# Optimization experiments

Hardware: AMD Instinct MI355X
Metric: run time of the kernel (lower is better)

Reference implementation:

```python
import jax, jax.numpy as jnp
import numpy as np

B, N, C = 2, 4096, 1024
H, WIN = 16, 20
D = C // H

def setup_inputs() -> dict:
    key = jax.random.key(0)
    ks = jax.random.split(key, 9)
    s = 1.0 / np.sqrt(C)
    d = {"q": jax.random.normal(ks[0], (B, N, C), jnp.float32)}
    for i, name in enumerate(["Wq", "Wk", "Wv", "Wo"]):
        d[name + "_w"] = jax.random.normal(ks[1 + 2 * i], (C, C), jnp.float32) * s
        d[name + "_b"] = jax.random.normal(ks[2 + 2 * i], (C,), jnp.float32) * 0.01
    return d

def reference(q, Wq_w, Wq_b, Wk_w, Wk_b, Wv_w, Wv_b, Wo_w, Wo_b):
    b, n, c = q.shape
    w2 = WIN // 2  # half window = 10
    def proj(x, w, bias):
        return (x @ w.T + bias).reshape(b, n, H, D).transpose(0, 2, 1, 3)  # [B,H,N,D]
    Q = proj(q, Wq_w, Wq_b)
    K = proj(q, Wk_w, Wk_b)
    V = proj(q, Wv_w, Wv_b)
    off = jnp.arange(-w2, w2 + 1)                       # [Wn] = 21 offsets
    pos = jnp.arange(n)[:, None] + off[None, :]         # [N, Wn] key index per query
    valid = (pos >= 0) & (pos < n)                      # edge clipping == torch start/end slicing
    idx = jnp.clip(pos, 0, n - 1)
    Kw = K[:, :, idx, :]                                # [B,H,N,Wn,D] gathered key windows
    Vw = V[:, :, idx, :]
    scale = jnp.sqrt(jnp.float32(D))
    scores = jnp.einsum('bhnd,bhnwd->bhnw', Q, Kw) / scale
    scores = jnp.where(valid[None, None], scores, -jnp.inf)
    probs = jax.nn.softmax(scores, axis=-1)             # invalid slots get exactly 0
    out = jnp.einsum('bhnw,bhnwd->bhnd', probs, Vw)
    out = out.transpose(0, 2, 1, 3).reshape(b, n, c)
    out = out @ Wo_w.T + Wo_b
    # torch returns attn_probs of the LAST loop iteration i=N-1: window [N-1-w2, N), size w2+1
    attn_last = probs[:, :, -1:, : w2 + 1]              # [B,H,1,11]
    return (out, attn_last)
```

## Files before the change

kernel.cpp:

```cpp
#include <hip/hip_runtime.h>
#include <hip/hip_bf16.h>

#define Bb 2
#define Nn 4096
#define Cc 1024
#define Hh 16
#define Dd 64
#define Mm (Bb*Nn)
#define W2 10
#define WINSZ 21

typedef __attribute__((ext_vector_type(8))) short  bf16x8s;
typedef __attribute__((ext_vector_type(4))) float  f32x4;
typedef __attribute__((ext_vector_type(4))) unsigned short us4;

#define AS1 __attribute__((address_space(1)))
#define AS3 __attribute__((address_space(3)))

__device__ __forceinline__ unsigned short f2bf(float f) {
  unsigned int u = __float_as_uint(f);
  u += 0x7FFFu + ((u >> 16) & 1u);
  return (unsigned short)(u >> 16);
}
__device__ __forceinline__ float bflo(unsigned int u) { return __uint_as_float(u << 16); }
__device__ __forceinline__ float bfhi(unsigned int u) { return __uint_as_float(u & 0xFFFF0000u); }

__device__ __forceinline__ us4 cvt4(float4 v) {
  us4 o;
  o.x = f2bf(v.x); o.y = f2bf(v.y); o.z = f2bf(v.z); o.w = f2bf(v.w);
  return o;
}

__global__ __launch_bounds__(256) void cvt_all(const float4* __restrict__ q,
                                               const float4* __restrict__ wq,
                                               const float4* __restrict__ wk,
                                               const float4* __restrict__ wv,
                                               const float4* __restrict__ wo,
                                               const float* __restrict__ bq,
                                               const float* __restrict__ bk,
                                               const float* __restrict__ bv,
                                               us4* __restrict__ qb4,
                                               us4* __restrict__ wqkv4,
                                               us4* __restrict__ wo4,
                                               float* __restrict__ bqkv) {
  const int NQ = 2097152, NW = 262144, TOT = NQ + 4 * NW;
  const int gid = blockIdx.x * 256 + threadIdx.x;
  const int stride = gridDim.x * 256;
  for (int i = gid; i < TOT; i += stride) {
    if (i < NQ) {
      qb4[i] = cvt4(q[i]);
    } else {
      int j = i - NQ;
      int r = j >> 18, k = j & (NW - 1);
      if (r == 0)      wqkv4[k]          = cvt4(wq[k]);
      else if (r == 1) wqkv4[NW + k]     = cvt4(wk[k]);
      else if (r == 2) wqkv4[2 * NW + k] = cvt4(wv[k]);
      else             wo4[k]            = cvt4(wo[k]);
    }
  }
  if (gid < 3072) {
    float v = (gid < 1024) ? bq[gid] : (gid < 2048) ? bk[gid - 1024] : bv[gid - 2048];
    bqkv[gid] = v;
  }
}

template<bool OUT_BF16>
__global__ __launch_bounds__(512) void gemm_k32(const unsigned short* __restrict__ A,
                                                const unsigned short* __restrict__ Bm,
                                                const float* __restrict__ bias,
                                                void* __restrict__ Cout,
                                                int N) {
  constexpr int K = 1024, NT = 32;
  __shared__ unsigned short lds[3][12288];

  const int tid = threadIdx.x, wid = tid >> 6, lane = tid & 63;
  const int wm = wid >> 2, wn = wid & 3;

  const int nwg = gridDim.x, cpx = nwg >> 3, bid = blockIdx.x;
  const int swz = (bid & 7) * cpx + (bid >> 3);
  const int nbn = N >> 8;
  const int m0 = (swz / nbn) << 7, n0 = (swz % nbn) << 8;

  const unsigned short* aS  = A  + (size_t)(m0 + wid * 16 + (lane >> 2)) * K + (lane & 3) * 8;
  const unsigned short* bS0 = Bm + (size_t)(n0 + wid * 32 + (lane >> 2)) * K + (lane & 3) * 8;
  const unsigned short* bS1 = bS0 + (size_t)16 * K;
  const int dA = wid * 512, dB0 = 4096 + wid * 1024, dB1 = 4096 + wid * 1024 + 512;

#define STG(bf, kt) do {                                                                      \
    const size_t ko = (size_t)(kt) * 32;                                                      \
    __builtin_amdgcn_global_load_lds((AS1 const void*)(aS  + ko), (AS3 void*)(&lds[bf][dA ]), 16, 0, 0); \
    __builtin_amdgcn_global_load_lds((AS1 const void*)(bS0 + ko), (AS3 void*)(&lds[bf][dB0]), 16, 0, 0); \
    __builtin_amdgcn_global_load_lds((AS1 const void*)(bS1 + ko), (AS3 void*)(&lds[bf][dB1]), 16, 0, 0); \
  } while (0)

  int aoff[4], boff[4];
#pragma unroll
  for (int f = 0; f < 4; ++f) {
    aoff[f] = (wm * 64 + f * 16 + (lane & 15)) * 32 + (lane >> 4) * 8;
    boff[f] = 4096 + (wn * 64 + f * 16 + (lane & 15)) * 32 + (lane >> 4) * 8;
  }

  f32x4 acc[4][4] = {};

  STG(0, 0);
  STG(1, 1);
  asm volatile("s_waitcnt vmcnt(3)" ::: "memory");
  __builtin_amdgcn_sched_barrier(0);
  __builtin_amdgcn_s_barrier();
  __builtin_amdgcn_sched_barrier(0);

#pragma unroll 4
  for (int t = 0; t < NT; ++t) {
    const int cur = t % 3;
    if (t + 2 < NT) STG((t + 2) % 3, t + 2);

    const unsigned short* L = &lds[cur][0];
    bf16x8s a[4], b[4];
#pragma unroll
    for (int f = 0; f < 4; ++f) a[f] = *(const bf16x8s*)(L + aoff[f]);
#pragma unroll
    for (int f = 0; f < 4; ++f) b[f] = *(const bf16x8s*)(L + boff[f]);
    __builtin_amdgcn_s_setprio(1);
#pragma unroll
    for (int fm = 0; fm < 4; ++fm)
#pragma unroll
      for (int fn = 0; fn < 4; ++fn)
        acc[fm][fn] = __builtin_amdgcn_mfma_f32_16x16x32_bf16(a[fm], b[fn], acc[fm][fn], 0, 0, 0);
    __builtin_amdgcn_s_setprio(0);

    if (t + 1 < NT) {
      if (t + 2 < NT) asm volatile("s_waitcnt vmcnt(3)" ::: "memory");
      else            asm volatile("s_waitcnt vmcnt(0)" ::: "memory");
      __builtin_amdgcn_sched_barrier(0);
      __builtin_amdgcn_s_barrier();
      __builtin_amdgcn_sched_barrier(0);
    }
  }
#undef STG

  const int r0 = m0 + wm * 64 + (lane >> 4) * 4;
  const int c0 = n0 + wn * 64 + (lane & 15);
#pragma unroll
  for (int fm = 0; fm < 4; ++fm) {
#pragma unroll
    for (int fn = 0; fn < 4; ++fn) {
      const int col = c0 + fn * 16;
      const float bv = bias[col];
#pragma unroll
      for (int r = 0; r < 4; ++r) {
        const int row = r0 + fm * 16 + r;
        const float v = acc[fm][fn][r] + bv;
        if (OUT_BF16)
          ((unsigned short*)Cout)[(size_t)row * N + col] = f2bf(v);
        else
          ((float*)Cout)[(size_t)row * N + col] = v;
      }
    }
  }
}

#define TN 128
#define KVROWS (TN + 2 * W2)

__global__ void attn_kernel(const unsigned short* __restrict__ QKV,
                            unsigned short* __restrict__ AO,
                            float* __restrict__ attn_last) {
  __shared__ uint4 Kl[KVROWS * 8];
  __shared__ uint4 Vl[KVROWS * 8];

  const int nt = Nn / TN;
  const int bid = blockIdx.x;
  const int tile = bid & (nt - 1);
  const int bh = bid / nt;
  const int h = bh & (Hh - 1), b = bh / Hh;
  const int n0 = tile * TN;
  const int tid = threadIdx.x;

  for (int idx = tid; idx < KVROWS * 8; idx += 256) {
    const int r = idx >> 3, c = idx & 7;
    const int pos = n0 - W2 + r;
    uint4 kv = make_uint4(0, 0, 0, 0), vv = make_uint4(0, 0, 0, 0);
    if (pos >= 0 && pos < Nn) {
      const uint4* row = (const uint4*)(QKV + (size_t)(b * Nn + pos) * 3072);
      kv = row[128 + h * 8 + c];
      vv = row[256 + h * 8 + c];
    }
    const int slot = c ^ (r & 7);
    Kl[r * 8 + slot] = kv;
    Vl[r * 8 + slot] = vv;
  }
  __syncthreads();

  const int row  = tid >> 1;
  const int half = tid & 1;
  const int n = n0 + row;
  const size_t m = (size_t)b * Nn + n;

  const uint4* qrow = (const uint4*)(QKV + m * 3072) + h * 8 + half * 4;
  const uint4 qd0 = qrow[0], qd1 = qrow[1], qd2 = qrow[2], qd3 = qrow[3];

  float p[WINSZ];
#pragma unroll
  for (int w = 0; w < WINSZ; ++w) p[w] = 0.f;

#pragma unroll
  for (int c = 0; c < 4; ++c) {
    const uint4 qv = (c == 0) ? qd0 : (c == 1) ? qd1 : (c == 2) ? qd2 : qd3;
    const float q0 = bflo(qv.x), q1 = bfhi(qv.x);
    const float q2 = bflo(qv.y), q3 = bfhi(qv.y);
    const float q4 = bflo(qv.z), q5 = bfhi(qv.z);
    const float q6 = bflo(qv.w), q7 = bfhi(qv.w);
#pragma unroll 7
    for (int w = 0; w < WINSZ; ++w) {
      const int r = row + w;
      const uint4 v = Kl[r * 8 + ((half * 4 + c) ^ (r & 7))];
      float a0 = q0 * bflo(v.x);
      float a1 = q1 * bfhi(v.x);
      a0 += q2 * bflo(v.y);
      a1 += q3 * bfhi(v.y);
      a0 += q4 * bflo(v.z);
      a1 += q5 * bfhi(v.z);
      a0 += q6 * bflo(v.w);
      a1 += q7 * bfhi(v.w);
      p[w] += a0 + a1;
    }
  }

#pragma unroll
  for (int w = 0; w < WINSZ; ++w) {
    float t = p[w];
    t += __shfl_xor(t, 1, 64);
    const int pos = n - W2 + w;
    p[w] = (pos < 0 || pos >= Nn) ? -1e30f : t * 0.125f;
  }
  float mx = p[0];
#pragma unroll
  for (int w = 1; w < WINSZ; ++w) mx = fmaxf(mx, p[w]);
  float sum = 0.f;
#pragma unroll
  for (int w = 0; w < WINSZ; ++w) { p[w] = __expf(p[w] - mx); sum += p[w]; }
  const float inv = 1.0f / sum;

  if (n == Nn - 1 && half == 0) {
#pragma unroll
    for (int w = 0; w <= W2; ++w)
      attn_last[(b * Hh + h) * (W2 + 1) + w] = p[w] * inv;
  }

  uint4* orow = (uint4*)(AO + m * Cc + h * Dd) + half * 4;
#pragma unroll
  for (int c = 0; c < 4; ++c) {
    float o0 = 0.f, o1 = 0.f, o2 = 0.f, o3 = 0.f;
    float o4 = 0.f, o5 = 0.f, o6 = 0.f, o7 = 0.f;
#pragma unroll 7
    for (int w = 0; w < WINSZ; ++w) {
      const int r = row + w;
      const uint4 v = Vl[r * 8 + ((half * 4 + c) ^ (r & 7))];
      const float pw = p[w];
      o0 += pw * bflo(v.x);
      o1 += pw * bfhi(v.x);
      o2 += pw * bflo(v.y);
      o3 += pw * bfhi(v.y);
      o4 += pw * bflo(v.z);
      o5 += pw * bfhi(v.z);
      o6 += pw * bflo(v.w);
      o7 += pw * bfhi(v.w);
    }
    unsigned int d0 = (unsigned int)f2bf(o0 * inv) | ((unsigned int)f2bf(o1 * inv) << 16);
    unsigned int d1 = (unsigned int)f2bf(o2 * inv) | ((unsigned int)f2bf(o3 * inv) << 16);
    unsigned int d2 = (unsigned int)f2bf(o4 * inv) | ((unsigned int)f2bf(o5 * inv) << 16);
    unsigned int d3 = (unsigned int)f2bf(o6 * inv) | ((unsigned int)f2bf(o7 * inv) << 16);
    orow[c] = make_uint4(d0, d1, d2, d3);
  }
}

extern "C" void kernel_launch(void* const* d_in, const int* in_sizes, int n_in,
                              void* d_out, int out_size, void* d_ws, size_t ws_size,
                              hipStream_t stream) {
  const float* q    = (const float*)d_in[0];
  const float* Wq_w = (const float*)d_in[1];
  const float* Wq_b = (const float*)d_in[2];
  const float* Wk_w = (const float*)d_in[3];
  const float* Wk_b = (const float*)d_in[4];
  const float* Wv_w = (const float*)d_in[5];
  const float* Wv_b = (const float*)d_in[6];
  const float* Wo_w = (const float*)d_in[7];
  const float* Wo_b = (const float*)d_in[8];
  float* out = (float*)d_out;
  float* attn_last = out + (size_t)Mm * Cc;

  char* ws = (char*)d_ws;
  unsigned short* qb   = (unsigned short*)(ws);
  unsigned short* Wqkv = (unsigned short*)(ws + 16777216);
  unsigned short* Wo16 = (unsigned short*)(ws + 16777216 + 6291456);
  float*          bqkv = (float*)(ws + 25165824);
  unsigned short* QKV  = (unsigned short*)(ws + 25182208);
  unsigned short* AO   = (unsigned short*)(ws + 75513856);

  cvt_all<<<2048, 256, 0, stream>>>((const float4*)q,
                                    (const float4*)Wq_w, (const float4*)Wk_w,
                                    (const float4*)Wv_w, (const float4*)Wo_w,
                                    Wq_b, Wk_b, Wv_b,
                                    (us4*)qb, (us4*)Wqkv, (us4*)Wo16, bqkv);

  {
    dim3 grid((Mm / 128) * (3072 / 256));
    gemm_k32<true><<<grid, 512, 0, stream>>>(qb, Wqkv, bqkv, (void*)QKV, 3072);
  }

  {
    dim3 grid(Bb * Hh * (Nn / TN));
    attn_kernel<<<grid, 256, 0, stream>>>(QKV, AO, attn_last);
  }

  {
    dim3 grid((Mm / 128) * (Cc / 256));
    gemm_k32<false><<<grid, 512, 0, stream>>>(AO, Wo16, Wo_b, (void*)out, Cc);
  }
}
```

Measured before the change: 145.9 us.

## Replace GEMM with 256x256-tile, K64, XOR-swizzled, 8-phase pipelined kernel

Rewrites both projection GEMMs to use 256x256 output tiles with K-step 64, double-buffered 128KB LDS staging and XOR-swizzled chunk placement to avoid bank conflicts. The main loop interleaves partial LDS reads, global-to-LDS prefetches and MFMA bursts in an 8-phase schedule with barriers and priority hints. Larger tiles aim to raise arithmetic intensity and MFMA utilisation. The cost is more accumulator registers, fewer workgroups (the output GEMM drops to 128 blocks, fewer than the CU count), and many barriers per iteration.

After: 145.8 us. About the same (-0.0%).

```diff
diff --git a/kernel.cpp b/kernel.cpp
--- a/kernel.cpp
+++ b/kernel.cpp
@@ -65,83 +65,99 @@
 }
 
 template<bool OUT_BF16>
-__global__ __launch_bounds__(512) void gemm_k32(const unsigned short* __restrict__ A,
-                                                const unsigned short* __restrict__ Bm,
-                                                const float* __restrict__ bias,
-                                                void* __restrict__ Cout,
-                                                int N) {
-  constexpr int K = 1024, NT = 32;
-  __shared__ unsigned short lds[3][12288];
+__global__ __launch_bounds__(512) void gemm8p(const unsigned short* __restrict__ A,
+                                              const unsigned short* __restrict__ Bm,
+                                              const float* __restrict__ bias,
+                                              void* __restrict__ Cout,
+                                              int N) {
+  constexpr int K = 1024;
+  __shared__ unsigned short lds[65536];
 
   const int tid = threadIdx.x, wid = tid >> 6, lane = tid & 63;
   const int wm = wid >> 2, wn = wid & 3;
 
   const int nwg = gridDim.x, cpx = nwg >> 3, bid = blockIdx.x;
   const int swz = (bid & 7) * cpx + (bid >> 3);
-  const int nbn = N >> 8;
-  const int m0 = (swz / nbn) << 7, n0 = (swz % nbn) << 8;
-
-  const unsigned short* aS  = A  + (size_t)(m0 + wid * 16 + (lane >> 2)) * K + (lane & 3) * 8;
-  const unsigned short* bS0 = Bm + (size_t)(n0 + wid * 32 + (lane >> 2)) * K + (lane & 3) * 8;
-  const unsigned short* bS1 = bS0 + (size_t)16 * K;
-  const int dA = wid * 512, dB0 = 4096 + wid * 1024, dB1 = 4096 + wid * 1024 + 512;
-
-#define STG(bf, kt) do {                                                                      \
-    const size_t ko = (size_t)(kt) * 32;                                                      \
-    __builtin_amdgcn_global_load_lds((AS1 const void*)(aS  + ko), (AS3 void*)(&lds[bf][dA ]), 16, 0, 0); \
-    __builtin_amdgcn_global_load_lds((AS1 const void*)(bS0 + ko), (AS3 void*)(&lds[bf][dB0]), 16, 0, 0); \
-    __builtin_amdgcn_global_load_lds((AS1 const void*)(bS1 + ko), (AS3 void*)(&lds[bf][dB1]), 16, 0, 0); \
-  } while (0)
-
-  int aoff[4], boff[4];
-#pragma unroll
-  for (int f = 0; f < 4; ++f) {
-    aoff[f] = (wm * 64 + f * 16 + (lane & 15)) * 32 + (lane >> 4) * 8;
-    boff[f] = 4096 + (wn * 64 + f * 16 + (lane & 15)) * 32 + (lane >> 4) * 8;
-  }
-
-  f32x4 acc[4][4] = {};
-
-  STG(0, 0);
-  STG(1, 1);
-  asm volatile("s_waitcnt vmcnt(3)" ::: "memory");
-  __builtin_amdgcn_sched_barrier(0);
-  __builtin_amdgcn_s_barrier();
-  __builtin_amdgcn_sched_barrier(0);
-
-#pragma unroll 4
-  for (int t = 0; t < NT; ++t) {
-    const int cur = t % 3;
-    if (t + 2 < NT) STG((t + 2) % 3, t + 2);
-
-    const unsigned short* L = &lds[cur][0];
-    bf16x8s a[4], b[4];
-#pragma unroll
-    for (int f = 0; f < 4; ++f) a[f] = *(const bf16x8s*)(L + aoff[f]);
-#pragma unroll
-    for (int f = 0; f < 4; ++f) b[f] = *(const bf16x8s*)(L + boff[f]);
-    __builtin_amdgcn_s_setprio(1);
-#pragma unroll
-    for (int fm = 0; fm < 4; ++fm)
-#pragma unroll
-      for (int fn = 0; fn < 4; ++fn)
-        acc[fm][fn] = __builtin_amdgcn_mfma_f32_16x16x32_bf16(a[fm], b[fn], acc[fm][fn], 0, 0, 0);
-    __builtin_amdgcn_s_setprio(0);
-
-    if (t + 1 < NT) {
-      if (t + 2 < NT) asm volatile("s_waitcnt vmcnt(3)" ::: "memory");
-      else            asm volatile("s_waitcnt vmcnt(0)" ::: "memory");
-      __builtin_amdgcn_sched_barrier(0);
-      __builtin_amdgcn_s_barrier();
-      __builtin_amdgcn_sched_barrier(0);
-    }
-  }
-#undef STG
-
-  const int r0 = m0 + wm * 64 + (lane >> 4) * 4;
+  constexpr int NBM = Mm / 256;
+  const int m0 = (swz % NBM) << 8, n0 = (swz / NBM) << 8;
+
+  const int rbase = wid * 8 + (lane >> 3);
+  const int cst = ((lane & 7) ^ (lane >> 3)) * 8;
+  const unsigned short* aP0 = A  + (size_t)(m0 + rbase) * K + cst;
+  const unsigned short* aP1 = aP0 + (size_t)128 * K;
+  const unsigned short* bP0 = Bm + (size_t)(n0 + rbase) * K + cst;
+  const unsigned short* bP1 = bP0 + (size_t)128 * K;
+
+  const int awb = wm * 8192 + (lane & 15) * 64;
+  const int bwb = 16384 + (wn >> 1) * 8192 + (wn & 1) * 4096 + (lane & 15) * 64;
+  const int chs0 = (((lane >> 4)) ^ (lane & 7)) * 8;
+  const int chs1 = ((4 + (lane >> 4)) ^ (lane & 7)) * 8;
+
+  f32x4 acc[8][4] = {};
+  bf16x8s breg[4][2], areg[2][2];
+
+#define GL(sp, off) __builtin_amdgcn_global_load_lds((AS1 const void*)(sp), (AS3 void*)(&lds[off]), 16, 0, 0)
+#define STGA(d,h,kt) do { const unsigned short* _s = ((h) ? aP1 : aP0) + (size_t)(kt) * 64; \
+    GL(_s,                   (d)*32768 + (h)*8192 +        wid*512); \
+    GL(_s + (size_t)64 * K,  (d)*32768 + (h)*8192 + 4096 + wid*512); } while (0)
+#define STGB(d,h,kt) do { const unsigned short* _s = ((h) ? bP1 : bP0) + (size_t)(kt) * 64; \
+    GL(_s,                   (d)*32768 + 16384 + (h)*8192 +        wid*512); \
+    GL(_s + (size_t)64 * K,  (d)*32768 + 16384 + (h)*8192 + 4096 + wid*512); } while (0)
+#define LDB(d) do { _Pragma("unroll") for (int fn = 0; fn < 4; ++fn) { \
+    breg[fn][0] = *(const bf16x8s*)(&lds[(d)*32768 + bwb + fn*1024 + chs0]); \
+    breg[fn][1] = *(const bf16x8s*)(&lds[(d)*32768 + bwb + fn*1024 + chs1]); } } while (0)
+#define LDA(d,q) do { _Pragma("unroll") for (int u = 0; u < 2; ++u) { \
+    areg[u][0] = *(const bf16x8s*)(&lds[(d)*32768 + awb + ((q)*2+u)*1024 + chs0]); \
+    areg[u][1] = *(const bf16x8s*)(&lds[(d)*32768 + awb + ((q)*2+u)*1024 + chs1]); } } while (0)
+#define MF16(q) do { _Pragma("unroll") for (int u = 0; u < 2; ++u) _Pragma("unroll") for (int fn = 0; fn < 4; ++fn) { \
+    acc[(q)*2+u][fn] = __builtin_amdgcn_mfma_f32_16x16x32_bf16(areg[u][0], breg[fn][0], acc[(q)*2+u][fn], 0, 0, 0); \
+    acc[(q)*2+u][fn] = __builtin_amdgcn_mfma_f32_16x16x32_bf16(areg[u][1], breg[fn][1], acc[(q)*2+u][fn], 0, 0, 0); } } while (0)
+#define SB __builtin_amdgcn_sched_barrier(0)
+#define BAR __builtin_amdgcn_s_barrier()
+#define LGKM0 asm volatile("s_waitcnt lgkmcnt(0)" ::: "memory")
+#define PRIO1 __builtin_amdgcn_s_setprio(1)
+#define PRIO0 __builtin_amdgcn_s_setprio(0)
+
+  STGA(0,0,0); STGA(0,1,0); STGB(0,0,0); STGB(0,1,0);
+  STGA(1,0,1); STGA(1,1,1); STGB(1,0,1); STGB(1,1,1);
+  asm volatile("s_waitcnt vmcnt(8)" ::: "memory");
+  SB; BAR; SB;
+
+#pragma unroll 1
+  for (int j = 0; j < 8; ++j) {
+    const int tA1 = 2*j + 1;
+    const int t0  = (2*j + 2) & 15;
+    const int tB1 = (2*j + 3) & 15;
+    LDB(0); LDA(0,0); STGA(1,0,tA1);          SB; BAR; LGKM0; SB;
+    PRIO1; MF16(0); PRIO0; SB; BAR; SB;
+    LDA(0,1); STGA(1,1,tA1); STGB(0,0,t0);    SB; BAR; LGKM0; SB;
+    PRIO1; MF16(1); PRIO0; SB; BAR; SB;
+    LDA(0,2); STGB(0,1,t0);                   SB; BAR; LGKM0; SB;
+    PRIO1; MF16(2); PRIO0; SB; BAR; SB;
+    LDA(0,3);                                 SB; BAR; LGKM0; SB;
+    PRIO1; MF16(3); PRIO0; SB;
+    asm volatile("s_waitcnt vmcnt(4)" ::: "memory"); SB; BAR; SB;
+    LDB(1); LDA(1,0); STGA(0,0,t0);           SB; BAR; LGKM0; SB;
+    PRIO1; MF16(0); PRIO0; SB; BAR; SB;
+    LDA(1,1); STGA(0,1,t0); STGB(1,0,tB1);    SB; BAR; LGKM0; SB;
+    PRIO1; MF16(1); PRIO0; SB; BAR; SB;
+    LDA(1,2); STGB(1,1,tB1);                  SB; BAR; LGKM0; SB;
+    PRIO1; MF16(2); PRIO0; SB; BAR; SB;
+    LDA(1,3);                                 SB; BAR; LGKM0; SB;
+    PRIO1; MF16(3); PRIO0; SB;
+    asm volatile("s_waitcnt vmcnt(4)" ::: "memory"); SB; BAR; SB;
+  }
+#undef GL
+#undef STGA
+#undef STGB
+#undef LDB
+#undef LDA
+#undef MF16
+
+  const int r0 = m0 + wm * 128 + (lane >> 4) * 4;
   const int c0 = n0 + wn * 64 + (lane & 15);
 #pragma unroll
-  for (int fm = 0; fm < 4; ++fm) {
+  for (int fm = 0; fm < 8; ++fm) {
 #pragma unroll
     for (int fn = 0; fn < 4; ++fn) {
       const int col = c0 + fn * 16;
@@ -304,8 +320,8 @@
                                     (us4*)qb, (us4*)Wqkv, (us4*)Wo16, bqkv);
 
   {
-    dim3 grid((Mm / 128) * (3072 / 256));
-    gemm_k32<true><<<grid, 512, 0, stream>>>(qb, Wqkv, bqkv, (void*)QKV, 3072);
+    dim3 grid((Mm / 256) * (3072 / 256));
+    gemm8p<true><<<grid, 512, 0, stream>>>(qb, Wqkv, bqkv, (void*)QKV, 3072);
   }
 
   {
@@ -314,7 +330,7 @@
   }
 
   {
-    dim3 grid((Mm / 128) * (Cc / 256));
-    gemm_k32<false><<<grid, 512, 0, stream>>>(AO, Wo16, Wo_b, (void*)out, Cc);
-  }
-}
+    dim3 grid((Mm / 256) * (Cc / 256));
+    gemm8p<false><<<grid, 512, 0, stream>>>(AO, Wo16, Wo_b, (void*)out, Cc);
+  }
+}
```

## Switch GEMMs to 128x128 tiles with 256 threads and XOR-swizzled LDS layout

Applied to the files above, without the earlier changes.

Both projection GEMMs move from 128x256 tiles on 512-thread blocks to 128x128 tiles on 256-thread blocks, with a 2x2 wave layout and M-major block ordering. The global-to-LDS staging now uses an XOR swizzle on the 16-byte column group, and the fragment reads apply the same swizzle, to cut LDS bank conflicts. The ring-buffer indices are tracked incrementally with unroll 1 instead of modulo arithmetic. Smaller tiles give more blocks and smaller LDS use per block, at the cost of less operand reuse per block.

New measurement: 151.6 us. 1.04x slower.

```diff
diff --git a/kernel.cpp b/kernel.cpp
--- a/kernel.cpp
+++ b/kernel.cpp
@@ -65,54 +65,59 @@
 }
 
 template<bool OUT_BF16>
-__global__ __launch_bounds__(512) void gemm_k32(const unsigned short* __restrict__ A,
-                                                const unsigned short* __restrict__ Bm,
-                                                const float* __restrict__ bias,
-                                                void* __restrict__ Cout,
-                                                int N) {
+__global__ __launch_bounds__(256) void gemm_mb(const unsigned short* __restrict__ A,
+                                               const unsigned short* __restrict__ Bm,
+                                               const float* __restrict__ bias,
+                                               void* __restrict__ Cout,
+                                               int N) {
   constexpr int K = 1024, NT = 32;
-  __shared__ unsigned short lds[3][12288];
+  __shared__ unsigned short lds[3][8192];
 
   const int tid = threadIdx.x, wid = tid >> 6, lane = tid & 63;
-  const int wm = wid >> 2, wn = wid & 3;
+  const int wm = wid >> 1, wn = wid & 1;
 
   const int nwg = gridDim.x, cpx = nwg >> 3, bid = blockIdx.x;
   const int swz = (bid & 7) * cpx + (bid >> 3);
-  const int nbn = N >> 8;
-  const int m0 = (swz / nbn) << 7, n0 = (swz % nbn) << 8;
-
-  const unsigned short* aS  = A  + (size_t)(m0 + wid * 16 + (lane >> 2)) * K + (lane & 3) * 8;
-  const unsigned short* bS0 = Bm + (size_t)(n0 + wid * 32 + (lane >> 2)) * K + (lane & 3) * 8;
-  const unsigned short* bS1 = bS0 + (size_t)16 * K;
-  const int dA = wid * 512, dB0 = 4096 + wid * 1024, dB1 = 4096 + wid * 1024 + 512;
-
-#define STG(bf, kt) do {                                                                      \
-    const size_t ko = (size_t)(kt) * 32;                                                      \
-    __builtin_amdgcn_global_load_lds((AS1 const void*)(aS  + ko), (AS3 void*)(&lds[bf][dA ]), 16, 0, 0); \
-    __builtin_amdgcn_global_load_lds((AS1 const void*)(bS0 + ko), (AS3 void*)(&lds[bf][dB0]), 16, 0, 0); \
-    __builtin_amdgcn_global_load_lds((AS1 const void*)(bS1 + ko), (AS3 void*)(&lds[bf][dB1]), 16, 0, 0); \
+  constexpr int NBM = Mm / 128;
+  const int m0 = (swz % NBM) << 7, n0 = (swz / NBM) << 7;
+
+  const int srow = tid >> 2;
+  const int g = (tid & 3) ^ (srow & 3) ^ ((srow >> 2) & 3);
+  const unsigned short* aS0 = A  + (size_t)(m0 + srow) * K + g * 8;
+  const unsigned short* aS1 = aS0 + (size_t)64 * K;
+  const unsigned short* bS0 = Bm + (size_t)(n0 + srow) * K + g * 8;
+  const unsigned short* bS1 = bS0 + (size_t)64 * K;
+  const int d0 = wid * 512;
+
+#define STG(bf, kt) do {                                                                    \
+    const size_t ko = (size_t)(kt) * 32;                                                    \
+    __builtin_amdgcn_global_load_lds((AS1 const void*)(aS0 + ko), (AS3 void*)(&lds[bf][       d0]), 16, 0, 0); \
+    __builtin_amdgcn_global_load_lds((AS1 const void*)(aS1 + ko), (AS3 void*)(&lds[bf][2048 + d0]), 16, 0, 0); \
+    __builtin_amdgcn_global_load_lds((AS1 const void*)(bS0 + ko), (AS3 void*)(&lds[bf][4096 + d0]), 16, 0, 0); \
+    __builtin_amdgcn_global_load_lds((AS1 const void*)(bS1 + ko), (AS3 void*)(&lds[bf][6144 + d0]), 16, 0, 0); \
   } while (0)
 
+  const int slot8 = (((lane >> 4) ^ (lane & 3) ^ ((lane >> 2) & 3))) * 8;
   int aoff[4], boff[4];
 #pragma unroll
   for (int f = 0; f < 4; ++f) {
-    aoff[f] = (wm * 64 + f * 16 + (lane & 15)) * 32 + (lane >> 4) * 8;
-    boff[f] = 4096 + (wn * 64 + f * 16 + (lane & 15)) * 32 + (lane >> 4) * 8;
+    aoff[f] = (wm * 64 + f * 16 + (lane & 15)) * 32 + slot8;
+    boff[f] = 4096 + (wn * 64 + f * 16 + (lane & 15)) * 32 + slot8;
   }
 
   f32x4 acc[4][4] = {};
 
   STG(0, 0);
   STG(1, 1);
-  asm volatile("s_waitcnt vmcnt(3)" ::: "memory");
+  asm volatile("s_waitcnt vmcnt(4)" ::: "memory");
   __builtin_amdgcn_sched_barrier(0);
   __builtin_amdgcn_s_barrier();
   __builtin_amdgcn_sched_barrier(0);
 
-#pragma unroll 4
+  int cur = 0, stg = 2;
+#pragma unroll 1
   for (int t = 0; t < NT; ++t) {
-    const int cur = t % 3;
-    if (t + 2 < NT) STG((t + 2) % 3, t + 2);
+    if (t + 2 < NT) STG(stg, t + 2);
 
     const unsigned short* L = &lds[cur][0];
     bf16x8s a[4], b[4];
@@ -129,12 +134,14 @@
     __builtin_amdgcn_s_setprio(0);
 
     if (t + 1 < NT) {
-      if (t + 2 < NT) asm volatile("s_waitcnt vmcnt(3)" ::: "memory");
+      if (t + 2 < NT) asm volatile("s_waitcnt vmcnt(4)" ::: "memory");
       else            asm volatile("s_waitcnt vmcnt(0)" ::: "memory");
       __builtin_amdgcn_sched_barrier(0);
       __builtin_amdgcn_s_barrier();
       __builtin_amdgcn_sched_barrier(0);
     }
+    cur = (cur == 2) ? 0 : cur + 1;
+    stg = (stg == 2) ? 0 : stg + 1;
   }
 #undef STG
 
@@ -304,8 +311,8 @@
                                     (us4*)qb, (us4*)Wqkv, (us4*)Wo16, bqkv);
 
   {
-    dim3 grid((Mm / 128) * (3072 / 256));
-    gemm_k32<true><<<grid, 512, 0, stream>>>(qb, Wqkv, bqkv, (void*)QKV, 3072);
+    dim3 grid((Mm / 128) * (3072 / 128));
+    gemm_mb<true><<<grid, 256, 0, stream>>>(qb, Wqkv, bqkv, (void*)QKV, 3072);
   }
 
   {
@@ -314,7 +321,7 @@
   }
 
   {
-    dim3 grid((Mm / 128) * (Cc / 256));
-    gemm_k32<false><<<grid, 512, 0, stream>>>(AO, Wo16, Wo_b, (void*)out, Cc);
-  }
-}
+    dim3 grid((Mm / 128) * (Cc / 128));
+    gemm_mb<false><<<grid, 256, 0, stream>>>(AO, Wo16, Wo_b, (void*)out, Cc);
+  }
+}
```

## Swizzle GEMM LDS layout and split attention rows across four threads

Applied to the files above, without the earlier changes.

The GEMM's global-to-LDS staging now uses an XOR swizzle on the 16-byte chunk index, with matching swizzled read offsets. This is meant to cut LDS bank conflicts when fragments are loaded, and it also changes how the B tile rows are laid out in LDS. The attention kernel goes from 256 to 512 threads, with each query row split across four lanes instead of two and an extra shuffle reduction. This raises parallelism and lowers per-thread register pressure, at the cost of more redundant softmax work and shuffles.

Result: faster. 140.0 us (-4.0%).

```diff
diff --git a/kernel.cpp b/kernel.cpp
--- a/kernel.cpp
+++ b/kernel.cpp
@@ -81,10 +81,12 @@
   const int nbn = N >> 8;
   const int m0 = (swz / nbn) << 7, n0 = (swz % nbn) << 8;
 
-  const unsigned short* aS  = A  + (size_t)(m0 + wid * 16 + (lane >> 2)) * K + (lane & 3) * 8;
-  const unsigned short* bS0 = Bm + (size_t)(n0 + wid * 32 + (lane >> 2)) * K + (lane & 3) * 8;
-  const unsigned short* bS1 = bS0 + (size_t)16 * K;
-  const int dA = wid * 512, dB0 = 4096 + wid * 1024, dB1 = 4096 + wid * 1024 + 512;
+  const int srow = wid * 16 + (lane >> 2);
+  const int g8 = ((lane & 3) ^ ((lane >> 3) & 3)) * 8;
+  const unsigned short* aS  = A  + (size_t)(m0 + srow) * K + g8;
+  const unsigned short* bS0 = Bm + (size_t)(n0 + srow) * K + g8;
+  const unsigned short* bS1 = Bm + (size_t)(n0 + 128 + srow) * K + g8;
+  const int dA = wid * 512, dB0 = 4096 + wid * 512, dB1 = 8192 + wid * 512;
 
 #define STG(bf, kt) do {                                                                      \
     const size_t ko = (size_t)(kt) * 32;                                                      \
@@ -93,11 +95,12 @@
     __builtin_amdgcn_global_load_lds((AS1 const void*)(bS1 + ko), (AS3 void*)(&lds[bf][dB1]), 16, 0, 0); \
   } while (0)
 
+  const int slot8 = ((lane >> 4) ^ (((lane & 15) >> 1) & 3)) * 8;
   int aoff[4], boff[4];
 #pragma unroll
   for (int f = 0; f < 4; ++f) {
-    aoff[f] = (wm * 64 + f * 16 + (lane & 15)) * 32 + (lane >> 4) * 8;
-    boff[f] = 4096 + (wn * 64 + f * 16 + (lane & 15)) * 32 + (lane >> 4) * 8;
+    aoff[f] = (wm * 64 + f * 16 + (lane & 15)) * 32 + slot8;
+    boff[f] = 4096 + (wn * 64 + f * 16 + (lane & 15)) * 32 + slot8;
   }
 
   f32x4 acc[4][4] = {};
@@ -162,9 +165,9 @@
 #define TN 128
 #define KVROWS (TN + 2 * W2)
 
-__global__ void attn_kernel(const unsigned short* __restrict__ QKV,
-                            unsigned short* __restrict__ AO,
-                            float* __restrict__ attn_last) {
+__global__ __launch_bounds__(512) void attn_kernel(const unsigned short* __restrict__ QKV,
+                                                   unsigned short* __restrict__ AO,
+                                                   float* __restrict__ attn_last) {
   __shared__ uint4 Kl[KVROWS * 8];
   __shared__ uint4 Vl[KVROWS * 8];
 
@@ -176,7 +179,7 @@
   const int n0 = tile * TN;
   const int tid = threadIdx.x;
 
-  for (int idx = tid; idx < KVROWS * 8; idx += 256) {
+  for (int idx = tid; idx < KVROWS * 8; idx += 512) {
     const int r = idx >> 3, c = idx & 7;
     const int pos = n0 - W2 + r;
     uint4 kv = make_uint4(0, 0, 0, 0), vv = make_uint4(0, 0, 0, 0);
@@ -191,21 +194,21 @@
   }
   __syncthreads();
 
-  const int row  = tid >> 1;
-  const int half = tid & 1;
+  const int row = tid >> 2;
+  const int qtr = tid & 3;
   const int n = n0 + row;
   const size_t m = (size_t)b * Nn + n;
 
-  const uint4* qrow = (const uint4*)(QKV + m * 3072) + h * 8 + half * 4;
-  const uint4 qd0 = qrow[0], qd1 = qrow[1], qd2 = qrow[2], qd3 = qrow[3];
+  const uint4* qrow = (const uint4*)(QKV + m * 3072) + h * 8 + qtr * 2;
+  const uint4 qd0 = qrow[0], qd1 = qrow[1];
 
   float p[WINSZ];
 #pragma unroll
   for (int w = 0; w < WINSZ; ++w) p[w] = 0.f;
 
 #pragma unroll
-  for (int c = 0; c < 4; ++c) {
-    const uint4 qv = (c == 0) ? qd0 : (c == 1) ? qd1 : (c == 2) ? qd2 : qd3;
+  for (int c = 0; c < 2; ++c) {
+    const uint4 qv = (c == 0) ? qd0 : qd1;
     const float q0 = bflo(qv.x), q1 = bfhi(qv.x);
     const float q2 = bflo(qv.y), q3 = bfhi(qv.y);
     const float q4 = bflo(qv.z), q5 = bfhi(qv.z);
@@ -213,7 +216,7 @@
 #pragma unroll 7
     for (int w = 0; w < WINSZ; ++w) {
       const int r = row + w;
-      const uint4 v = Kl[r * 8 + ((half * 4 + c) ^ (r & 7))];
+      const uint4 v = Kl[r * 8 + ((qtr * 2 + c) ^ (r & 7))];
       float a0 = q0 * bflo(v.x);
       float a1 = q1 * bfhi(v.x);
       a0 += q2 * bflo(v.y);
@@ -230,6 +233,7 @@
   for (int w = 0; w < WINSZ; ++w) {
     float t = p[w];
     t += __shfl_xor(t, 1, 64);
+    t += __shfl_xor(t, 2, 64);
     const int pos = n - W2 + w;
     p[w] = (pos < 0 || pos >= Nn) ? -1e30f : t * 0.125f;
   }
@@ -241,21 +245,21 @@
   for (int w = 0; w < WINSZ; ++w) { p[w] = __expf(p[w] - mx); sum += p[w]; }
   const float inv = 1.0f / sum;
 
-  if (n == Nn - 1 && half == 0) {
+  if (n == Nn - 1 && qtr == 0) {
 #pragma unroll
     for (int w = 0; w <= W2; ++w)
       attn_last[(b * Hh + h) * (W2 + 1) + w] = p[w] * inv;
   }
 
-  uint4* orow = (uint4*)(AO + m * Cc + h * Dd) + half * 4;
-#pragma unroll
-  for (int c = 0; c < 4; ++c) {
+  uint4* orow = (uint4*)(AO + m * Cc + h * Dd) + qtr * 2;
+#pragma unroll
+  for (int c = 0; c < 2; ++c) {
     float o0 = 0.f, o1 = 0.f, o2 = 0.f, o3 = 0.f;
     float o4 = 0.f, o5 = 0.f, o6 = 0.f, o7 = 0.f;
 #pragma unroll 7
     for (int w = 0; w < WINSZ; ++w) {
       const int r = row + w;
-      const uint4 v = Vl[r * 8 + ((half * 4 + c) ^ (r & 7))];
+      const uint4 v = Vl[r * 8 + ((qtr * 2 + c) ^ (r & 7))];
       const float pw = p[w];
       o0 += pw * bflo(v.x);
       o1 += pw * bfhi(v.x);
@@ -310,7 +314,7 @@
 
   {
     dim3 grid(Bb * Hh * (Nn / TN));
-    attn_kernel<<<grid, 256, 0, stream>>>(QKV, AO, attn_last);
+    attn_kernel<<<grid, 512, 0, stream>>>(QKV, AO, attn_last);
   }
 
   {
```
